# Kernel tuning notes

Measured on AMD Instinct MI355X. Metric: run time of the kernel, lower is better.

## Reference

```python
import jax, jax.numpy as jnp
import numpy as np

EMBED_DIM = 1024
NUM_HEADS = 16
HEAD_DIM = EMBED_DIM // NUM_HEADS
LN_EPS = 1e-5


def setup_inputs() -> dict:
    key = jax.random.key(0)
    ks = jax.random.split(key, 10)
    B, S, D = 1, 4096, EMBED_DIM
    s = 1.0 / np.sqrt(D)
    inp = {
        'input': jax.random.normal(ks[0], (B, S, D), dtype=jnp.float32),
        'Wq': jax.random.normal(ks[1], (D, D), dtype=jnp.float32) * s,
        'bq': jnp.zeros((D,), dtype=jnp.float32),
        'Wk': jax.random.normal(ks[2], (D, D), dtype=jnp.float32) * s,
        'bk': jnp.zeros((D,), dtype=jnp.float32),
        'Wv': jax.random.normal(ks[3], (D, D), dtype=jnp.float32) * s,
        'bv': jnp.zeros((D,), dtype=jnp.float32),
        'Wo': jax.random.normal(ks[4], (D, D), dtype=jnp.float32) * s,
        'bo': jnp.zeros((D,), dtype=jnp.float32),
        'ln_gamma': jnp.ones((D,), dtype=jnp.float32),
        'ln_beta': jnp.zeros((D,), dtype=jnp.float32),
    }
    return inp


def reference(input, Wq, bq, Wk, bk, Wv, bv, Wo, bo, ln_gamma, ln_beta):
    B, S, D = input.shape
    H, Hd = NUM_HEADS, HEAD_DIM
    # projections (torch Linear: x @ W.T + b)
    q = input @ Wq.T + bq
    k = input @ Wk.T + bk
    v = input @ Wv.T + bv
    # [B, H, S, Hd]
    q = q.reshape(B, S, H, Hd).transpose(0, 2, 1, 3)
    k = k.reshape(B, S, H, Hd).transpose(0, 2, 1, 3)
    v = v.reshape(B, S, H, Hd).transpose(0, 2, 1, 3)
    scores = jnp.einsum('bhqd,bhkd->bhqk', q, k) / jnp.sqrt(jnp.float32(Hd))
    causal = jnp.tril(jnp.ones((S, S), dtype=bool))  # [S, S]
    scores = jnp.where(causal[None, None, :, :], scores, -jnp.inf)
    attn = jax.nn.softmax(scores, axis=-1)  # stable (max-subtract) internally
    out = jnp.einsum('bhqk,bhkd->bhqd', attn, v)
    out = out.transpose(0, 2, 1, 3).reshape(B, S, D)
    out = out @ Wo.T + bo
    out = out + input
    # LayerNorm
    mu = jnp.mean(out, axis=-1, keepdims=True)
    var = jnp.var(out, axis=-1, keepdims=True)
    normed = (out - mu) * jax.lax.rsqrt(var + LN_EPS)
    return normed * ln_gamma + ln_beta
```

## Files before the change

### kernel.cpp

```cpp
#include <hip/hip_runtime.h>
#include <hip/hip_bf16.h>

typedef float floatx4 __attribute__((ext_vector_type(4)));
typedef short short8 __attribute__((ext_vector_type(8)));

#define S_LEN 4096
#define D_DIM 1024
#define NHEAD 16
#define SCALE_LOG2 0.1803368801111204f

__device__ __forceinline__ void gload_lds16(const void* g, void* l) {
  __builtin_amdgcn_global_load_lds(
      (const __attribute__((address_space(1))) unsigned int*)g,
      (__attribute__((address_space(3))) unsigned int*)l, 16, 0, 0);
}

__device__ __forceinline__ unsigned short f2bf_bits(float f) {
  __hip_bfloat16 h = __float2bfloat16(f);
  return __builtin_bit_cast(unsigned short, h);
}

__global__ __launch_bounds__(256) void cvt_f32_bf16(const float* __restrict__ in,
                                                    unsigned short* __restrict__ out,
                                                    int n4) {
  int i = blockIdx.x * 256 + threadIdx.x;
  if (i >= n4) return;
  float4 v = reinterpret_cast<const float4*>(in)[i];
  ushort4 u;
  u.x = f2bf_bits(v.x);
  u.y = f2bf_bits(v.y);
  u.z = f2bf_bits(v.z);
  u.w = f2bf_bits(v.w);
  reinterpret_cast<ushort4*>(out)[i] = u;
}

__global__ __launch_bounds__(256) void cvt4_f32_bf16(const float* __restrict__ w0,
                                                     const float* __restrict__ w1,
                                                     const float* __restrict__ w2,
                                                     const float* __restrict__ w3,
                                                     unsigned short* __restrict__ o0,
                                                     unsigned short* __restrict__ o1,
                                                     unsigned short* __restrict__ o2,
                                                     unsigned short* __restrict__ o3) {
  const int which = blockIdx.x >> 10;
  const int i = (blockIdx.x & 1023) * 256 + threadIdx.x;
  const float* in = which == 0 ? w0 : which == 1 ? w1 : which == 2 ? w2 : w3;
  unsigned short* out = which == 0 ? o0 : which == 1 ? o1 : which == 2 ? o2 : o3;
  float4 v = reinterpret_cast<const float4*>(in)[i];
  ushort4 u;
  u.x = f2bf_bits(v.x);
  u.y = f2bf_bits(v.y);
  u.z = f2bf_bits(v.z);
  u.w = f2bf_bits(v.w);
  reinterpret_cast<ushort4*>(out)[i] = u;
}

__global__ __launch_bounds__(256) void gemm_qkv(const unsigned short* __restrict__ A,
                                                const unsigned short* __restrict__ WqB,
                                                const unsigned short* __restrict__ WkB,
                                                const unsigned short* __restrict__ WvB,
                                                const float* __restrict__ bq,
                                                const float* __restrict__ bk,
                                                const float* __restrict__ bv,
                                                unsigned short* __restrict__ Qo,
                                                unsigned short* __restrict__ Ko,
                                                unsigned short* __restrict__ VTo) {
  __shared__ __align__(16) unsigned short As[128 * 32];
  __shared__ __align__(16) unsigned short Bs[128 * 32];
  const int K = 1024, N = 1024, M = 4096;
  const int tid = threadIdx.x;
  const int wave = tid >> 6, lane = tid & 63;
  const int seg = blockIdx.y >> 3;
  const int m0 = blockIdx.x * 128, n0 = (blockIdx.y & 7) * 128;
  const unsigned short* B = seg == 0 ? WqB : seg == 1 ? WkB : WvB;
  const float* bias = seg == 0 ? bq : seg == 1 ? bk : bv;
  const int wr = wave >> 1, wc = wave & 1;

  floatx4 acc[4][4] = {};
  const unsigned short* Ab = A + (size_t)m0 * K;
  const unsigned short* Bb = B + (size_t)n0 * K;
  const int srow = lane >> 2, scol = (lane & 3) * 8;
  const int aRow = lane & 15, kOff = (lane >> 4) * 8;

  for (int k0 = 0; k0 < K; k0 += 32) {
#pragma unroll
    for (int i = 0; i < 2; ++i) {
      const int c = wave * 2 + i;
      const int row = c * 16 + srow;
      gload_lds16(Ab + (size_t)row * K + k0 + scol, &As[c * 512]);
      gload_lds16(Bb + (size_t)row * K + k0 + scol, &Bs[c * 512]);
    }
    __syncthreads();
    short8 af[4], bfg[4];
#pragma unroll
    for (int f = 0; f < 4; ++f) {
      af[f] = *reinterpret_cast<const short8*>(&As[(wr * 64 + f * 16 + aRow) * 32 + kOff]);
      bfg[f] = *reinterpret_cast<const short8*>(&Bs[(wc * 64 + f * 16 + aRow) * 32 + kOff]);
    }
#pragma unroll
    for (int fm = 0; fm < 4; ++fm)
#pragma unroll
      for (int fn = 0; fn < 4; ++fn)
        acc[fm][fn] =
            __builtin_amdgcn_mfma_f32_16x16x32_bf16(af[fm], bfg[fn], acc[fm][fn], 0, 0, 0);
    __syncthreads();
  }

  const int rb = (lane >> 4) * 4, cl = lane & 15;
  const float osc = seg == 0 ? SCALE_LOG2 : 1.0f;
#pragma unroll
  for (int fm = 0; fm < 4; ++fm)
#pragma unroll
    for (int fn = 0; fn < 4; ++fn)
#pragma unroll
      for (int r = 0; r < 4; ++r) {
        const int row = m0 + wr * 64 + fm * 16 + rb + r;
        const int col = n0 + wc * 64 + fn * 16 + cl;
        const float v = (acc[fm][fn][r] + bias[col]) * osc;
        if (seg == 0)
          Qo[(size_t)row * N + col] = f2bf_bits(v);
        else if (seg == 1)
          Ko[(size_t)row * N + col] = f2bf_bits(v);
        else
          VTo[(size_t)col * M + row] = f2bf_bits(v);
      }
}

__global__ __launch_bounds__(256) void gemm_o(const unsigned short* __restrict__ A,
                                              const unsigned short* __restrict__ B,
                                              const float* __restrict__ bias,
                                              const float* __restrict__ resid,
                                              float* __restrict__ C) {
  __shared__ __align__(16) unsigned short As[64 * 32];
  __shared__ __align__(16) unsigned short Bs[128 * 32];
  const int K = 1024, N = 1024;
  const int tid = threadIdx.x;
  const int wave = tid >> 6, lane = tid & 63;
  const int m0 = blockIdx.x * 64, n0 = blockIdx.y * 128;
  const int wr = wave >> 1, wc = wave & 1;

  floatx4 acc[2][4] = {};
  const unsigned short* Ab = A + (size_t)m0 * K;
  const unsigned short* Bb = B + (size_t)n0 * K;
  const int srow = lane >> 2, scol = (lane & 3) * 8;
  const int aRow = lane & 15, kOff = (lane >> 4) * 8;

  for (int k0 = 0; k0 < K; k0 += 32) {
#pragma unroll
    for (int i = 0; i < 3; ++i) {
      const int ci = wave * 3 + i;
      if (ci < 4) {
        const int row = ci * 16 + srow;
        gload_lds16(Ab + (size_t)row * K + k0 + scol, &As[ci * 512]);
      } else {
        const int row = (ci - 4) * 16 + srow;
        gload_lds16(Bb + (size_t)row * K + k0 + scol, &Bs[(ci - 4) * 512]);
      }
    }
    __syncthreads();
    short8 af[2], bfg[4];
#pragma unroll
    for (int f = 0; f < 2; ++f)
      af[f] = *reinterpret_cast<const short8*>(&As[(wr * 32 + f * 16 + aRow) * 32 + kOff]);
#pragma unroll
    for (int f = 0; f < 4; ++f)
      bfg[f] = *reinterpret_cast<const short8*>(&Bs[(wc * 64 + f * 16 + aRow) * 32 + kOff]);
#pragma unroll
    for (int fm = 0; fm < 2; ++fm)
#pragma unroll
      for (int fn = 0; fn < 4; ++fn)
        acc[fm][fn] =
            __builtin_amdgcn_mfma_f32_16x16x32_bf16(af[fm], bfg[fn], acc[fm][fn], 0, 0, 0);
    __syncthreads();
  }

  const int rb = (lane >> 4) * 4, cl = lane & 15;
#pragma unroll
  for (int fm = 0; fm < 2; ++fm)
#pragma unroll
    for (int fn = 0; fn < 4; ++fn)
#pragma unroll
      for (int r = 0; r < 4; ++r) {
        const int row = m0 + wr * 32 + fm * 16 + rb + r;
        const int col = n0 + wc * 64 + fn * 16 + cl;
        C[(size_t)row * N + col] =
            acc[fm][fn][r] + bias[col] + resid[(size_t)row * N + col];
      }
}

__global__ __launch_bounds__(256) void attn_fwd(const unsigned short* __restrict__ Q,
                                                const unsigned short* __restrict__ Kg,
                                                const unsigned short* __restrict__ VT,
                                                unsigned short* __restrict__ O) {
  __shared__ __align__(16) unsigned short Ks[2 * 64 * 64];
  __shared__ __align__(16) unsigned short Vs[2 * 64 * 64];
  __shared__ __align__(16) unsigned short Ps[4][16 * 64];

  const int bid = blockIdx.x;
  const int h = bid & 15;
  const int pairIdx = bid >> 4;
  const int wave = threadIdx.x >> 6, lane = threadIdx.x & 63;
  const int l15 = lane & 15, l4 = lane >> 4;
  const int q7 = l15 & 7;

  auto stage = [&](int buf, int t) {
    const int kv0 = t * 64;
#pragma unroll
    for (int i = 0; i < 2; ++i) {
      const int seg = wave * 2 + i;
      const int c = seg * 64 + lane;
      const int r = c >> 3, jj = c & 7;
      const int sj = (jj ^ (r & 7)) * 8;
      gload_lds16(&Kg[(size_t)(kv0 + r) * D_DIM + h * 64 + sj],
                  &Ks[buf * 4096 + seg * 512]);
      gload_lds16(&VT[(size_t)(h * 64 + r) * S_LEN + kv0 + sj],
                  &Vs[buf * 4096 + seg * 512]);
    }
  };

  for (int ph = 0; ph < 2; ++ph) {
    const int qt = ph == 0 ? (63 - pairIdx) : pairIdx;
    const int q0 = qt * 64;
    const int qrow = q0 + wave * 16 + l15;

    short8 qf[2];
#pragma unroll
    for (int ks = 0; ks < 2; ++ks)
      qf[ks] = *reinterpret_cast<const short8*>(
          &Q[(size_t)qrow * D_DIM + h * 64 + ks * 32 + l4 * 8]);

    floatx4 acco[4] = {};
    float m_run = -1e30f, l_run = 0.f;

    const int ntiles = qt + 1;
    stage(0, 0);
    int cur = 0;
    for (int t = 0; t < ntiles; ++t) {
      if (t + 1 < ntiles) {
        stage(cur ^ 1, t + 1);
        asm volatile("s_waitcnt vmcnt(4)" ::: "memory");
      } else {
        asm volatile("s_waitcnt vmcnt(0)" ::: "memory");
      }
      __builtin_amdgcn_s_barrier();

      const unsigned short* ksb = &Ks[cur * 4096];
      const unsigned short* vsb = &Vs[cur * 4096];
      const int kv0 = t * 64;

      floatx4 accs[4] = {};
#pragma unroll
      for (int ks = 0; ks < 2; ++ks)
#pragma unroll
        for (int fn = 0; fn < 4; ++fn) {
          const int R = fn * 16 + l15;
          const int J = ks * 4 + l4;
          const short8 kf =
              *reinterpret_cast<const short8*>(&ksb[R * 64 + ((J ^ (R & 7)) * 8)]);
          accs[fn] =
              __builtin_amdgcn_mfma_f32_16x16x32_bf16(kf, qf[ks], accs[fn], 0, 0, 0);
        }

      float p[4][4];
#pragma unroll
      for (int fn = 0; fn < 4; ++fn)
#pragma unroll
        for (int r = 0; r < 4; ++r) p[fn][r] = accs[fn][r];

      if (t == ntiles - 1) {
#pragma unroll
        for (int fn = 0; fn < 4; ++fn)
#pragma unroll
          for (int r = 0; r < 4; ++r) {
            const int ka = kv0 + fn * 16 + l4 * 4 + r;
            p[fn][r] = (ka > qrow) ? -1e30f : p[fn][r];
          }
      }

      float mx = p[0][0];
#pragma unroll
      for (int fn = 0; fn < 4; ++fn)
#pragma unroll
        for (int r = 0; r < 4; ++r) mx = fmaxf(mx, p[fn][r]);
      mx = fmaxf(mx, __shfl_xor(mx, 16));
      mx = fmaxf(mx, __shfl_xor(mx, 32));

      if (!__all(mx <= m_run + 11.5f)) {
        const float mnew = fmaxf(m_run, mx);
        const float alpha = __builtin_amdgcn_exp2f(m_run - mnew);
        m_run = mnew;
        l_run *= alpha;
#pragma unroll
        for (int fn = 0; fn < 4; ++fn)
#pragma unroll
          for (int r = 0; r < 4; ++r) acco[fn][r] *= alpha;
      }

      float rs = 0.f;
#pragma unroll
      for (int fn = 0; fn < 4; ++fn)
#pragma unroll
        for (int r = 0; r < 4; ++r) {
          const float pv = __builtin_amdgcn_exp2f(p[fn][r] - m_run);
          p[fn][r] = pv;
          rs += pv;
        }
      l_run += rs;

#pragma unroll
      for (int fn = 0; fn < 4; ++fn) {
        const int c = 2 * fn + (l4 >> 1);
        const int off = ((c ^ q7) << 3) + ((l4 & 1) << 2);
        uint2 w;
        w.x = (unsigned)f2bf_bits(p[fn][0]) | ((unsigned)f2bf_bits(p[fn][1]) << 16);
        w.y = (unsigned)f2bf_bits(p[fn][2]) | ((unsigned)f2bf_bits(p[fn][3]) << 16);
        *reinterpret_cast<uint2*>(&Ps[wave][l15 * 64 + off]) = w;
      }

#pragma unroll
      for (int kh = 0; kh < 2; ++kh) {
        const short8 pf = *reinterpret_cast<const short8*>(
            &Ps[wave][l15 * 64 + (((kh * 4 + l4) ^ q7) << 3)]);
#pragma unroll
        for (int fn = 0; fn < 4; ++fn) {
          const int R = fn * 16 + l15;
          const int J = kh * 4 + l4;
          const short8 vf =
              *reinterpret_cast<const short8*>(&vsb[R * 64 + ((J ^ (R & 7)) * 8)]);
          acco[fn] = __builtin_amdgcn_mfma_f32_16x16x32_bf16(vf, pf, acco[fn], 0, 0, 0);
        }
      }
      __builtin_amdgcn_s_barrier();
      cur ^= 1;
    }

    l_run += __shfl_xor(l_run, 16);
    l_run += __shfl_xor(l_run, 32);
    const float inv = 1.f / l_run;
#pragma unroll
    for (int fn = 0; fn < 4; ++fn)
#pragma unroll
      for (int rp = 0; rp < 2; ++rp) {
        const unsigned lo = f2bf_bits(acco[fn][2 * rp] * inv);
        const unsigned hi = f2bf_bits(acco[fn][2 * rp + 1] * inv);
        *reinterpret_cast<unsigned*>(
            &O[(size_t)qrow * D_DIM + h * 64 + fn * 16 + l4 * 4 + rp * 2]) =
            lo | (hi << 16);
      }
  }
}

__global__ __launch_bounds__(256) void ln_kernel(const float* __restrict__ X,
                                                 const float* __restrict__ g,
                                                 const float* __restrict__ b,
                                                 float* __restrict__ Y) {
  const int row = blockIdx.x;
  const int t = threadIdx.x;
  const float4 xv = reinterpret_cast<const float4*>(X + (size_t)row * 1024)[t];
  float s = xv.x + xv.y + xv.z + xv.w;
  float s2 = xv.x * xv.x + xv.y * xv.y + xv.z * xv.z + xv.w * xv.w;
#pragma unroll
  for (int off = 1; off < 64; off <<= 1) {
    s += __shfl_xor(s, off);
    s2 += __shfl_xor(s2, off);
  }
  __shared__ float sr[4], sr2[4];
  const int wave = t >> 6, lane = t & 63;
  if (lane == 0) {
    sr[wave] = s;
    sr2[wave] = s2;
  }
  __syncthreads();
  const float S = sr[0] + sr[1] + sr[2] + sr[3];
  const float S2 = sr2[0] + sr2[1] + sr2[2] + sr2[3];
  const float mu = S * (1.f / 1024.f);
  const float var = S2 * (1.f / 1024.f) - mu * mu;
  const float rstd = rsqrtf(var + 1e-5f);
  const float4 gv = reinterpret_cast<const float4*>(g)[t];
  const float4 bv = reinterpret_cast<const float4*>(b)[t];
  float4 y;
  y.x = (xv.x - mu) * rstd * gv.x + bv.x;
  y.y = (xv.y - mu) * rstd * gv.y + bv.y;
  y.z = (xv.z - mu) * rstd * gv.z + bv.z;
  y.w = (xv.w - mu) * rstd * gv.w + bv.w;
  reinterpret_cast<float4*>(Y + (size_t)row * 1024)[t] = y;
}

extern "C" void kernel_launch(void* const* d_in, const int* in_sizes, int n_in,
                              void* d_out, int out_size, void* d_ws, size_t ws_size,
                              hipStream_t stream) {
  const float* x = (const float*)d_in[0];
  const float* Wq = (const float*)d_in[1];
  const float* bq = (const float*)d_in[2];
  const float* Wk = (const float*)d_in[3];
  const float* bk = (const float*)d_in[4];
  const float* Wv = (const float*)d_in[5];
  const float* bv = (const float*)d_in[6];
  const float* Wo = (const float*)d_in[7];
  const float* bo = (const float*)d_in[8];
  const float* gamma = (const float*)d_in[9];
  const float* beta = (const float*)d_in[10];

  char* ws = (char*)d_ws;
  const size_t MB = (size_t)1 << 20;
  unsigned short* Xb = (unsigned short*)(ws + 0);
  unsigned short* Wqb = (unsigned short*)(ws + 8 * MB);
  unsigned short* Wkb = (unsigned short*)(ws + 10 * MB);
  unsigned short* Wvb = (unsigned short*)(ws + 12 * MB);
  unsigned short* Wob = (unsigned short*)(ws + 16 * MB);
  unsigned short* Qb = (unsigned short*)(ws + 18 * MB);
  unsigned short* Kb = (unsigned short*)(ws + 26 * MB);
  unsigned short* VTb = (unsigned short*)(ws + 34 * MB);
  unsigned short* Ab = (unsigned short*)(ws + 42 * MB);
  float* proj = (float*)(ws + 0);

  cvt_f32_bf16<<<4096, 256, 0, stream>>>(x, Xb, 1048576);
  cvt4_f32_bf16<<<4096, 256, 0, stream>>>(Wq, Wk, Wv, Wo, Wqb, Wkb, Wvb, Wob);

  gemm_qkv<<<dim3(32, 24), 256, 0, stream>>>(Xb, Wqb, Wkb, Wvb, bq, bk, bv, Qb, Kb,
                                             VTb);

  attn_fwd<<<dim3(512), 256, 0, stream>>>(Qb, Kb, VTb, Ab);

  gemm_o<<<dim3(64, 8), 256, 0, stream>>>(Ab, Wob, bo, x, proj);

  ln_kernel<<<4096, 256, 0, stream>>>(proj, gamma, beta, (float*)d_out);
}
```

Measured before the change: 162.5 us.

## Merge conversion kernels, one q-tile per attention block, interleave P store with PV

The input and weight bf16 conversion kernels are merged into a single launch. The attention kernel drops the paired heavy/light q-tile scheme and launches 1024 blocks, each handling one q-tile with heavy tiles issued first. The P tile is now staged through LDS in 32-column halves interleaved with the PV MFMAs, which halves the P buffer. The row max is computed with a tree reduction instead of a serial chain. Removing the pairing gives more parallelism but relies on the hardware scheduler to balance the causal workload across blocks.

```diff
diff --git a/kernel.cpp b/kernel.cpp
--- a/kernel.cpp
+++ b/kernel.cpp
@@ -20,32 +20,30 @@
   return __builtin_bit_cast(unsigned short, h);
 }
 
-__global__ __launch_bounds__(256) void cvt_f32_bf16(const float* __restrict__ in,
-                                                    unsigned short* __restrict__ out,
-                                                    int n4) {
-  int i = blockIdx.x * 256 + threadIdx.x;
-  if (i >= n4) return;
-  float4 v = reinterpret_cast<const float4*>(in)[i];
-  ushort4 u;
-  u.x = f2bf_bits(v.x);
-  u.y = f2bf_bits(v.y);
-  u.z = f2bf_bits(v.z);
-  u.w = f2bf_bits(v.w);
-  reinterpret_cast<ushort4*>(out)[i] = u;
-}
-
-__global__ __launch_bounds__(256) void cvt4_f32_bf16(const float* __restrict__ w0,
-                                                     const float* __restrict__ w1,
-                                                     const float* __restrict__ w2,
-                                                     const float* __restrict__ w3,
-                                                     unsigned short* __restrict__ o0,
-                                                     unsigned short* __restrict__ o1,
-                                                     unsigned short* __restrict__ o2,
-                                                     unsigned short* __restrict__ o3) {
-  const int which = blockIdx.x >> 10;
-  const int i = (blockIdx.x & 1023) * 256 + threadIdx.x;
-  const float* in = which == 0 ? w0 : which == 1 ? w1 : which == 2 ? w2 : w3;
-  unsigned short* out = which == 0 ? o0 : which == 1 ? o1 : which == 2 ? o2 : o3;
+__global__ __launch_bounds__(256) void cvt_all(const float* __restrict__ x,
+                                               const float* __restrict__ w0,
+                                               const float* __restrict__ w1,
+                                               const float* __restrict__ w2,
+                                               const float* __restrict__ w3,
+                                               unsigned short* __restrict__ xo,
+                                               unsigned short* __restrict__ o0,
+                                               unsigned short* __restrict__ o1,
+                                               unsigned short* __restrict__ o2,
+                                               unsigned short* __restrict__ o3) {
+  const int bid = blockIdx.x;
+  const float* in;
+  unsigned short* out;
+  int i;
+  if (bid < 4096) {
+    in = x;
+    out = xo;
+    i = bid * 256 + threadIdx.x;
+  } else {
+    const int which = (bid - 4096) >> 10;
+    in = which == 0 ? w0 : which == 1 ? w1 : which == 2 ? w2 : w3;
+    out = which == 0 ? o0 : which == 1 ? o1 : which == 2 ? o2 : o3;
+    i = ((bid - 4096) & 1023) * 256 + threadIdx.x;
+  }
   float4 v = reinterpret_cast<const float4*>(in)[i];
   ushort4 u;
   u.x = f2bf_bits(v.x);
@@ -194,14 +192,25 @@
                                                 unsigned short* __restrict__ O) {
   __shared__ __align__(16) unsigned short Ks[2 * 64 * 64];
   __shared__ __align__(16) unsigned short Vs[2 * 64 * 64];
-  __shared__ __align__(16) unsigned short Ps[4][16 * 64];
+  __shared__ __align__(16) unsigned short Ps[4][16 * 32];
 
   const int bid = blockIdx.x;
   const int h = bid & 15;
-  const int pairIdx = bid >> 4;
+  const int qt = 63 - (bid >> 4);
+  const int q0 = qt * 64;
   const int wave = threadIdx.x >> 6, lane = threadIdx.x & 63;
   const int l15 = lane & 15, l4 = lane >> 4;
-  const int q7 = l15 & 7;
+  const int q3 = l15 & 3;
+
+  const int qrow = q0 + wave * 16 + l15;
+  short8 qf[2];
+#pragma unroll
+  for (int ks = 0; ks < 2; ++ks)
+    qf[ks] = *reinterpret_cast<const short8*>(
+        &Q[(size_t)qrow * D_DIM + h * 64 + ks * 32 + l4 * 8]);
+
+  floatx4 acco[4] = {};
+  float m_run = -1e30f, l_run = 0.f;
 
   auto stage = [&](int buf, int t) {
     const int kv0 = t * 64;
@@ -218,136 +227,124 @@
     }
   };
 
-  for (int ph = 0; ph < 2; ++ph) {
-    const int qt = ph == 0 ? (63 - pairIdx) : pairIdx;
-    const int q0 = qt * 64;
-    const int qrow = q0 + wave * 16 + l15;
-
-    short8 qf[2];
+  const int ntiles = qt + 1;
+  stage(0, 0);
+  int cur = 0;
+  for (int t = 0; t < ntiles; ++t) {
+    if (t + 1 < ntiles) {
+      stage(cur ^ 1, t + 1);
+      asm volatile("s_waitcnt vmcnt(4)" ::: "memory");
+    } else {
+      asm volatile("s_waitcnt vmcnt(0)" ::: "memory");
+    }
+    __builtin_amdgcn_s_barrier();
+
+    const unsigned short* ksb = &Ks[cur * 4096];
+    const unsigned short* vsb = &Vs[cur * 4096];
+    const int kv0 = t * 64;
+
+    floatx4 accs[4] = {};
 #pragma unroll
     for (int ks = 0; ks < 2; ++ks)
-      qf[ks] = *reinterpret_cast<const short8*>(
-          &Q[(size_t)qrow * D_DIM + h * 64 + ks * 32 + l4 * 8]);
-
-    floatx4 acco[4] = {};
-    float m_run = -1e30f, l_run = 0.f;
-
-    const int ntiles = qt + 1;
-    stage(0, 0);
-    int cur = 0;
-    for (int t = 0; t < ntiles; ++t) {
-      if (t + 1 < ntiles) {
-        stage(cur ^ 1, t + 1);
-        asm volatile("s_waitcnt vmcnt(4)" ::: "memory");
-      } else {
-        asm volatile("s_waitcnt vmcnt(0)" ::: "memory");
-      }
-      __builtin_amdgcn_s_barrier();
-
-      const unsigned short* ksb = &Ks[cur * 4096];
-      const unsigned short* vsb = &Vs[cur * 4096];
-      const int kv0 = t * 64;
-
-      floatx4 accs[4] = {};
-#pragma unroll
-      for (int ks = 0; ks < 2; ++ks)
-#pragma unroll
-        for (int fn = 0; fn < 4; ++fn) {
-          const int R = fn * 16 + l15;
-          const int J = ks * 4 + l4;
-          const short8 kf =
-              *reinterpret_cast<const short8*>(&ksb[R * 64 + ((J ^ (R & 7)) * 8)]);
-          accs[fn] =
-              __builtin_amdgcn_mfma_f32_16x16x32_bf16(kf, qf[ks], accs[fn], 0, 0, 0);
+#pragma unroll
+      for (int fn = 0; fn < 4; ++fn) {
+        const int R = fn * 16 + l15;
+        const int J = ks * 4 + l4;
+        const short8 kf =
+            *reinterpret_cast<const short8*>(&ksb[R * 64 + ((J ^ (R & 7)) * 8)]);
+        accs[fn] =
+            __builtin_amdgcn_mfma_f32_16x16x32_bf16(kf, qf[ks], accs[fn], 0, 0, 0);
+      }
+
+    float p[4][4];
+#pragma unroll
+    for (int fn = 0; fn < 4; ++fn)
+#pragma unroll
+      for (int r = 0; r < 4; ++r) p[fn][r] = accs[fn][r];
+
+    if (t == ntiles - 1) {
+#pragma unroll
+      for (int fn = 0; fn < 4; ++fn)
+#pragma unroll
+        for (int r = 0; r < 4; ++r) {
+          const int ka = kv0 + fn * 16 + l4 * 4 + r;
+          p[fn][r] = (ka > qrow) ? -1e30f : p[fn][r];
         }
-
-      float p[4][4];
+    }
+
+    const float a0 = fmaxf(fmaxf(p[0][0], p[0][1]), p[0][2]);
+    const float a1 = fmaxf(fmaxf(p[0][3], p[1][0]), p[1][1]);
+    const float a2 = fmaxf(fmaxf(p[1][2], p[1][3]), p[2][0]);
+    const float a3 = fmaxf(fmaxf(p[2][1], p[2][2]), p[2][3]);
+    const float a4 = fmaxf(fmaxf(p[3][0], p[3][1]), p[3][2]);
+    const float b0 = fmaxf(fmaxf(a0, a1), a2);
+    const float b1 = fmaxf(fmaxf(a3, a4), p[3][3]);
+    float mx = fmaxf(b0, b1);
+    mx = fmaxf(mx, __shfl_xor(mx, 16));
+    mx = fmaxf(mx, __shfl_xor(mx, 32));
+
+    if (!__all(mx <= m_run + 11.5f)) {
+      const float mnew = fmaxf(m_run, mx);
+      const float alpha = __builtin_amdgcn_exp2f(m_run - mnew);
+      m_run = mnew;
+      l_run *= alpha;
 #pragma unroll
       for (int fn = 0; fn < 4; ++fn)
 #pragma unroll
-        for (int r = 0; r < 4; ++r) p[fn][r] = accs[fn][r];
-
-      if (t == ntiles - 1) {
-#pragma unroll
-        for (int fn = 0; fn < 4; ++fn)
-#pragma unroll
-          for (int r = 0; r < 4; ++r) {
-            const int ka = kv0 + fn * 16 + l4 * 4 + r;
-            p[fn][r] = (ka > qrow) ? -1e30f : p[fn][r];
-          }
-      }
-
-      float mx = p[0][0];
-#pragma unroll
-      for (int fn = 0; fn < 4; ++fn)
-#pragma unroll
-        for (int r = 0; r < 4; ++r) mx = fmaxf(mx, p[fn][r]);
-      mx = fmaxf(mx, __shfl_xor(mx, 16));
-      mx = fmaxf(mx, __shfl_xor(mx, 32));
-
-      if (!__all(mx <= m_run + 11.5f)) {
-        const float mnew = fmaxf(m_run, mx);
-        const float alpha = __builtin_amdgcn_exp2f(m_run - mnew);
-        m_run = mnew;
-        l_run *= alpha;
-#pragma unroll
-        for (int fn = 0; fn < 4; ++fn)
-#pragma unroll
-          for (int r = 0; r < 4; ++r) acco[fn][r] *= alpha;
-      }
-
-      float rs = 0.f;
-#pragma unroll
-      for (int fn = 0; fn < 4; ++fn)
-#pragma unroll
-        for (int r = 0; r < 4; ++r) {
-          const float pv = __builtin_amdgcn_exp2f(p[fn][r] - m_run);
-          p[fn][r] = pv;
-          rs += pv;
-        }
-      l_run += rs;
-
-#pragma unroll
-      for (int fn = 0; fn < 4; ++fn) {
-        const int c = 2 * fn + (l4 >> 1);
-        const int off = ((c ^ q7) << 3) + ((l4 & 1) << 2);
+        for (int r = 0; r < 4; ++r) acco[fn][r] *= alpha;
+    }
+
+    float rs = 0.f;
+#pragma unroll
+    for (int fn = 0; fn < 4; ++fn)
+#pragma unroll
+      for (int r = 0; r < 4; ++r) {
+        const float pv = __builtin_amdgcn_exp2f(p[fn][r] - m_run);
+        p[fn][r] = pv;
+        rs += pv;
+      }
+    l_run += rs;
+
+#pragma unroll
+    for (int kh = 0; kh < 2; ++kh) {
+#pragma unroll
+      for (int b2 = 0; b2 < 2; ++b2) {
+        const int fn = 2 * kh + b2;
+        const int c = 2 * b2 + (l4 >> 1);
+        const int off = ((c ^ q3) << 3) + ((l4 & 1) << 2);
         uint2 w;
         w.x = (unsigned)f2bf_bits(p[fn][0]) | ((unsigned)f2bf_bits(p[fn][1]) << 16);
         w.y = (unsigned)f2bf_bits(p[fn][2]) | ((unsigned)f2bf_bits(p[fn][3]) << 16);
-        *reinterpret_cast<uint2*>(&Ps[wave][l15 * 64 + off]) = w;
-      }
-
-#pragma unroll
-      for (int kh = 0; kh < 2; ++kh) {
-        const short8 pf = *reinterpret_cast<const short8*>(
-            &Ps[wave][l15 * 64 + (((kh * 4 + l4) ^ q7) << 3)]);
-#pragma unroll
-        for (int fn = 0; fn < 4; ++fn) {
-          const int R = fn * 16 + l15;
-          const int J = kh * 4 + l4;
-          const short8 vf =
-              *reinterpret_cast<const short8*>(&vsb[R * 64 + ((J ^ (R & 7)) * 8)]);
-          acco[fn] = __builtin_amdgcn_mfma_f32_16x16x32_bf16(vf, pf, acco[fn], 0, 0, 0);
-        }
-      }
-      __builtin_amdgcn_s_barrier();
-      cur ^= 1;
-    }
-
-    l_run += __shfl_xor(l_run, 16);
-    l_run += __shfl_xor(l_run, 32);
-    const float inv = 1.f / l_run;
-#pragma unroll
-    for (int fn = 0; fn < 4; ++fn)
-#pragma unroll
-      for (int rp = 0; rp < 2; ++rp) {
-        const unsigned lo = f2bf_bits(acco[fn][2 * rp] * inv);
-        const unsigned hi = f2bf_bits(acco[fn][2 * rp + 1] * inv);
-        *reinterpret_cast<unsigned*>(
-            &O[(size_t)qrow * D_DIM + h * 64 + fn * 16 + l4 * 4 + rp * 2]) =
-            lo | (hi << 16);
-      }
-  }
+        *reinterpret_cast<uint2*>(&Ps[wave][l15 * 32 + off]) = w;
+      }
+      const short8 pf = *reinterpret_cast<const short8*>(
+          &Ps[wave][l15 * 32 + ((l4 ^ q3) << 3)]);
+#pragma unroll
+      for (int fn = 0; fn < 4; ++fn) {
+        const int R = fn * 16 + l15;
+        const int J = kh * 4 + l4;
+        const short8 vf =
+            *reinterpret_cast<const short8*>(&vsb[R * 64 + ((J ^ (R & 7)) * 8)]);
+        acco[fn] = __builtin_amdgcn_mfma_f32_16x16x32_bf16(vf, pf, acco[fn], 0, 0, 0);
+      }
+    }
+    __builtin_amdgcn_s_barrier();
+    cur ^= 1;
+  }
+
+  l_run += __shfl_xor(l_run, 16);
+  l_run += __shfl_xor(l_run, 32);
+  const float inv = 1.f / l_run;
+#pragma unroll
+  for (int fn = 0; fn < 4; ++fn)
+#pragma unroll
+    for (int rp = 0; rp < 2; ++rp) {
+      const unsigned lo = f2bf_bits(acco[fn][2 * rp] * inv);
+      const unsigned hi = f2bf_bits(acco[fn][2 * rp + 1] * inv);
+      *reinterpret_cast<unsigned*>(
+          &O[(size_t)qrow * D_DIM + h * 64 + fn * 16 + l4 * 4 + rp * 2]) =
+          lo | (hi << 16);
+    }
 }
 
 __global__ __launch_bounds__(256) void ln_kernel(const float* __restrict__ X,
@@ -414,13 +411,12 @@
   unsigned short* Ab = (unsigned short*)(ws + 42 * MB);
   float* proj = (float*)(ws + 0);
 
-  cvt_f32_bf16<<<4096, 256, 0, stream>>>(x, Xb, 1048576);
-  cvt4_f32_bf16<<<4096, 256, 0, stream>>>(Wq, Wk, Wv, Wo, Wqb, Wkb, Wvb, Wob);
+  cvt_all<<<8192, 256, 0, stream>>>(x, Wq, Wk, Wv, Wo, Xb, Wqb, Wkb, Wvb, Wob);
 
   gemm_qkv<<<dim3(32, 24), 256, 0, stream>>>(Xb, Wqb, Wkb, Wvb, bq, bk, bv, Qb, Kb,
                                              VTb);
 
-  attn_fwd<<<dim3(512), 256, 0, stream>>>(Qb, Kb, VTb, Ab);
+  attn_fwd<<<dim3(1024), 256, 0, stream>>>(Qb, Kb, VTb, Ab);
 
   gemm_o<<<dim3(64, 8), 256, 0, stream>>>(Ab, Wob, bo, x, proj);
 
```

Measured after the change: 162.7 us. Within noise of the previous version (+0.1%).
